# Kernel optimization log

Hardware: AMD Instinct MI355X
Metric: run time of the kernel (lower is better)

The kernel has to match this reference:

```python
import jax, jax.numpy as jnp
import numpy as np

N = 50000      # nodes
E = 800000     # edges (avg degree 16)
IN = 256       # in_features
HD = 4         # num_heads
D = 64         # out_features per head


def setup_inputs() -> dict:
    key = jax.random.key(0)
    k1, k2, k3, k4, k5 = jax.random.split(key, 5)
    h = jax.random.normal(k1, (N, IN), dtype=jnp.float32)
    edge_index = jax.random.randint(k2, (2, E), 0, N)
    # W stored as [in_features, num_heads*out_features] (h @ W == Linear(h))
    W = jax.random.normal(k3, (IN, HD * D), dtype=jnp.float32) * (1.0 / np.sqrt(IN))
    a_src = jax.random.normal(k4, (HD, D), dtype=jnp.float32) * 0.1
    a_dst = jax.random.normal(k5, (HD, D), dtype=jnp.float32) * 0.1
    return {"h": h, "edge_index": edge_index, "W": W, "a_src": a_src, "a_dst": a_dst}


def reference(h, edge_index, W, a_src, a_dst):
    n = h.shape[0]
    src, dst = edge_index[0], edge_index[1]
    # project: [N, H, D]
    hp = (h @ W).reshape(n, HD, D)
    # per-edge attention logits [E, H]
    e_src = jnp.einsum('ehd,hd->eh', hp[src], a_src)
    e_dst = jnp.einsum('ehd,hd->eh', hp[dst], a_dst)
    e = jax.nn.leaky_relu(e_src + e_dst, negative_slope=0.2)
    # segment softmax over incoming edges of each dst node
    e_max = jax.ops.segment_max(e, dst, num_segments=n)          # [N, H]
    ex = jnp.exp(e - e_max[dst])                                  # [E, H]
    e_sum = jax.ops.segment_sum(ex, dst, num_segments=n)         # [N, H]
    alpha = ex / (e_sum[dst] + 1e-16)                             # [E, H]
    # weighted aggregation
    msg = hp[src] * alpha[..., None]                              # [E, H, D]
    out = jax.ops.segment_sum(msg, dst, num_segments=n)          # [N, H, D]
    return out.reshape(n, HD * D)                                 # concat=True
```

## Files before the change

### kernel.cpp

```cpp
#include <hip/hip_runtime.h>

#define HD 4
#define D 64
#define NHD 256
#define N_IN 256

typedef __attribute__((ext_vector_type(8))) __bf16 bf16x8;
typedef __attribute__((ext_vector_type(4))) __bf16 bf16x4;
typedef __attribute__((ext_vector_type(4))) float f32x4;

constexpr int AROW = 40;

__global__ __launch_bounds__(256) void pre_kernel(const float* __restrict__ W,
                                                  __bf16* __restrict__ Wt,
                                                  const int* __restrict__ ei,
                                                  int* __restrict__ deg8, int Nn, int E) {
  const int b = blockIdx.x;
  if (b < N_IN) {
    const int k = b, n = threadIdx.x;
    Wt[n * N_IN + k] = (__bf16)W[k * NHD + n];
  } else {
    const int e = (b - N_IN) * 256 + threadIdx.x;
    const int c = b & 7;
    if (e < E) atomicAdd(&deg8[c * Nn + ei[E + e]], 1);
  }
}

__global__ __launch_bounds__(256) void gemm_scan_kernel(
    const float* __restrict__ A, const __bf16* __restrict__ Wt,
    const float* __restrict__ a_src, const float* __restrict__ a_dst,
    __bf16* __restrict__ hp16, float* __restrict__ s_out, float* __restrict__ t_out,
    int M, const int* __restrict__ deg8, int* __restrict__ partial,
    int* __restrict__ blocksum, int NB, int MT) {
  __shared__ __bf16 As[128 * AROW];
  __shared__ __bf16 Bs[128 * AROW];
  __shared__ int ws4[4];
  const int tid = threadIdx.x;

  if ((int)blockIdx.x < NB) {
    const int lane = tid & 63, wv = tid >> 6;
    const int base = blockIdx.x * 1024 + tid * 4;
    int v[4];
#pragma unroll
    for (int j = 0; j < 4; ++j) {
      int n = base + j;
      int sum = 0;
      if (n < M) {
#pragma unroll
        for (int c = 0; c < 8; ++c) sum += deg8[c * M + n];
      }
      v[j] = sum;
    }
    int sum = v[0] + v[1] + v[2] + v[3];
    int incl = sum;
#pragma unroll
    for (int off = 1; off < 64; off <<= 1) {
      int y = __shfl_up(incl, off);
      if (lane >= off) incl += y;
    }
    if (lane == 63) ws4[wv] = incl;
    __syncthreads();
    int wbase = 0;
#pragma unroll
    for (int w = 0; w < 4; ++w)
      if (w < wv) wbase += ws4[w];
    int excl = wbase + incl - sum;
    if (base + 0 < M) partial[base + 0] = excl;
    if (base + 1 < M) partial[base + 1] = excl + v[0];
    if (base + 2 < M) partial[base + 2] = excl + v[0] + v[1];
    if (base + 3 < M) partial[base + 3] = excl + v[0] + v[1] + v[2];
    if (tid == 255) blocksum[blockIdx.x] = wbase + incl;
    return;
  }

  const int g = blockIdx.x - NB;
  const int bx = g % MT, by = g / MT;
  const int lane = tid & 63, wv = tid >> 6;
  const int wr = wv >> 1, wc = wv & 1;
  const int c15 = lane & 15, quad = lane >> 4;
  const int m0 = bx * 128, n0 = by * 128;

  f32x4 acc[4][4];
#pragma unroll
  for (int i = 0; i < 4; ++i)
#pragma unroll
    for (int j = 0; j < 4; ++j) acc[i][j] = (f32x4){0.f, 0.f, 0.f, 0.f};

  const int am = tid >> 1, aks = (tid & 1) * 16;
  const int gr = m0 + am;
  const bool arow_ok = (gr < M);
  const float* Arow = &A[(size_t)gr * N_IN];
  const __bf16* Brow = &Wt[(size_t)(n0 + am) * N_IN];

  for (int kc = 0; kc < 8; ++kc) {
    const int k0 = kc * 32;
    float4 f0, f1, f2, f3;
    if (arow_ok) {
      f0 = *(const float4*)&Arow[k0 + aks + 0];
      f1 = *(const float4*)&Arow[k0 + aks + 4];
      f2 = *(const float4*)&Arow[k0 + aks + 8];
      f3 = *(const float4*)&Arow[k0 + aks + 12];
    } else {
      f0 = f1 = f2 = f3 = make_float4(0.f, 0.f, 0.f, 0.f);
    }
    bf16x8 b0 = *(const bf16x8*)&Brow[k0 + aks];
    bf16x8 b1 = *(const bf16x8*)&Brow[k0 + aks + 8];

    __syncthreads();
    bf16x8 a0, a1;
    a0[0] = (__bf16)f0.x; a0[1] = (__bf16)f0.y; a0[2] = (__bf16)f0.z; a0[3] = (__bf16)f0.w;
    a0[4] = (__bf16)f1.x; a0[5] = (__bf16)f1.y; a0[6] = (__bf16)f1.z; a0[7] = (__bf16)f1.w;
    a1[0] = (__bf16)f2.x; a1[1] = (__bf16)f2.y; a1[2] = (__bf16)f2.z; a1[3] = (__bf16)f2.w;
    a1[4] = (__bf16)f3.x; a1[5] = (__bf16)f3.y; a1[6] = (__bf16)f3.z; a1[7] = (__bf16)f3.w;
    *(bf16x8*)&As[am * AROW + aks + 0] = a0;
    *(bf16x8*)&As[am * AROW + aks + 8] = a1;
    *(bf16x8*)&Bs[am * AROW + aks + 0] = b0;
    *(bf16x8*)&Bs[am * AROW + aks + 8] = b1;
    __syncthreads();

    bf16x8 af[4], bf_[4];
#pragma unroll
    for (int i = 0; i < 4; ++i) {
      af[i]  = *(bf16x8*)&As[(wr * 64 + i * 16 + c15) * AROW + quad * 8];
      bf_[i] = *(bf16x8*)&Bs[(wc * 64 + i * 16 + c15) * AROW + quad * 8];
    }
#pragma unroll
    for (int mi = 0; mi < 4; ++mi)
#pragma unroll
      for (int ni = 0; ni < 4; ++ni)
        acc[mi][ni] = __builtin_amdgcn_mfma_f32_16x16x32_bf16(af[mi], bf_[ni], acc[mi][ni], 0, 0, 0);
  }

  const int head = by * 2 + wc;
  float av[4], ad[4];
#pragma unroll
  for (int ni = 0; ni < 4; ++ni) {
    av[ni] = a_src[head * D + ni * 16 + c15];
    ad[ni] = a_dst[head * D + ni * 16 + c15];
  }
  const int row0w = m0 + wr * 64;
#pragma unroll
  for (int mi = 0; mi < 4; ++mi) {
#pragma unroll
    for (int j = 0; j < 4; ++j) {
      float ps = acc[mi][0][j] * av[0] + acc[mi][1][j] * av[1] +
                 acc[mi][2][j] * av[2] + acc[mi][3][j] * av[3];
      float pt = acc[mi][0][j] * ad[0] + acc[mi][1][j] * ad[1] +
                 acc[mi][2][j] * ad[2] + acc[mi][3][j] * ad[3];
#pragma unroll
      for (int m = 1; m < 16; m <<= 1) {
        ps += __shfl_xor(ps, m);
        pt += __shfl_xor(pt, m);
      }
      const int row = row0w + mi * 16 + quad * 4 + j;
      if (c15 == 0 && row < M) {
        s_out[row * HD + head] = ps;
        t_out[row * HD + head] = pt;
      }
    }
#pragma unroll
    for (int ni = 0; ni < 4; ++ni) {
#pragma unroll
      for (int j = 0; j < 4; ++j) {
        const int row = row0w + mi * 16 + quad * 4 + j;
        const int col = n0 + wc * 64 + ni * 16 + c15;
        if (row < M) hp16[(size_t)row * NHD + col] = (__bf16)acc[mi][ni][j];
      }
    }
  }
}

__global__ __launch_bounds__(256) void scan23_kernel(const int* __restrict__ partial,
                                                     const int* __restrict__ blocksum,
                                                     const int* __restrict__ deg8,
                                                     int* __restrict__ row_ptr,
                                                     int* __restrict__ cursor8, int n, int NB) {
  __shared__ int s_off;
  const int tid = threadIdx.x;
  if (tid < 64) {
    int v = (tid < NB) ? blocksum[tid] : 0;
    int incl = v;
#pragma unroll
    for (int off = 1; off < 64; off <<= 1) {
      int y = __shfl_up(incl, off);
      if (tid >= off) incl += y;
    }
    int prev = __shfl_up(incl, 1);
    int excl = (tid == 0) ? 0 : prev;
    if (tid == (int)blockIdx.x) s_off = excl;
    if (blockIdx.x == 0 && tid == NB - 1) row_ptr[n] = incl;
  }
  __syncthreads();
  const int off = s_off;
  const int base = blockIdx.x * 1024 + tid * 4;
#pragma unroll
  for (int j = 0; j < 4; ++j) {
    const int node = base + j;
    if (node < n) {
      int rp = partial[node] + off;
      row_ptr[node] = rp;
      int run = rp;
#pragma unroll
      for (int c = 0; c < 8; ++c) {
        cursor8[c * n + node] = run;
        run += deg8[c * n + node];
      }
    }
  }
}

__global__ void scatter_kernel(const int* __restrict__ ei, int* __restrict__ cursor8,
                               int* __restrict__ csr_src, int Nn, int E) {
  int e = blockIdx.x * blockDim.x + threadIdx.x;
  if (e >= E) return;
  const int c = blockIdx.x & 7;
  int sn = ei[e], dn = ei[E + e];
  int pos = atomicAdd(&cursor8[c * Nn + dn], 1);
  csr_src[pos] = sn;
}

__global__ __launch_bounds__(256) void aggregate_kernel(
    const int* __restrict__ row_ptr, const int* __restrict__ csr_src,
    const float* __restrict__ s, const float* __restrict__ t,
    const __bf16* __restrict__ hp16, float* __restrict__ out, int N) {
  const int wave = threadIdx.x >> 6;
  const int lane = threadIdx.x & 63;
  const int node = blockIdx.x * 4 + wave;
  if (node >= N) return;
  const int h = lane >> 4;
  const int d0 = lane * 4;
  const int beg = row_ptr[node], end = row_ptr[node + 1];
  const float tn = t[node * HD + h];
  float num0 = 0.f, num1 = 0.f, num2 = 0.f, num3 = 0.f, den = 0.f;
  int i = beg;
  for (; i + 4 <= end; i += 4) {
    int sn0 = csr_src[i], sn1 = csr_src[i + 1], sn2 = csr_src[i + 2], sn3 = csr_src[i + 3];
    bf16x4 v0 = *(const bf16x4*)&hp16[(size_t)sn0 * NHD + d0];
    bf16x4 v1 = *(const bf16x4*)&hp16[(size_t)sn1 * NHD + d0];
    bf16x4 v2 = *(const bf16x4*)&hp16[(size_t)sn2 * NHD + d0];
    bf16x4 v3 = *(const bf16x4*)&hp16[(size_t)sn3 * NHD + d0];
    float lg0 = s[sn0 * HD + h] + tn;
    float lg1 = s[sn1 * HD + h] + tn;
    float lg2 = s[sn2 * HD + h] + tn;
    float lg3 = s[sn3 * HD + h] + tn;
    lg0 = fmaxf(lg0, 0.2f * lg0);
    lg1 = fmaxf(lg1, 0.2f * lg1);
    lg2 = fmaxf(lg2, 0.2f * lg2);
    lg3 = fmaxf(lg3, 0.2f * lg3);
    float ex0 = __expf(lg0), ex1 = __expf(lg1), ex2 = __expf(lg2), ex3 = __expf(lg3);
    den += (ex0 + ex1) + (ex2 + ex3);
    num0 += ex0 * (float)v0[0] + ex1 * (float)v1[0] + ex2 * (float)v2[0] + ex3 * (float)v3[0];
    num1 += ex0 * (float)v0[1] + ex1 * (float)v1[1] + ex2 * (float)v2[1] + ex3 * (float)v3[1];
    num2 += ex0 * (float)v0[2] + ex1 * (float)v1[2] + ex2 * (float)v2[2] + ex3 * (float)v3[2];
    num3 += ex0 * (float)v0[3] + ex1 * (float)v1[3] + ex2 * (float)v2[3] + ex3 * (float)v3[3];
  }
  for (; i < end; ++i) {
    int sn0 = csr_src[i];
    bf16x4 v0 = *(const bf16x4*)&hp16[(size_t)sn0 * NHD + d0];
    float lg0 = s[sn0 * HD + h] + tn;
    lg0 = fmaxf(lg0, 0.2f * lg0);
    float ex0 = __expf(lg0);
    den += ex0;
    num0 += ex0 * (float)v0[0];
    num1 += ex0 * (float)v0[1];
    num2 += ex0 * (float)v0[2];
    num3 += ex0 * (float)v0[3];
  }
  const float inv = 1.0f / (den + 1e-16f);
  float4 o = make_float4(num0 * inv, num1 * inv, num2 * inv, num3 * inv);
  *(float4*)&out[(size_t)node * NHD + d0] = o;
}

extern "C" void kernel_launch(void* const* d_in, const int* in_sizes, int n_in,
                              void* d_out, int out_size, void* d_ws, size_t ws_size,
                              hipStream_t stream) {
  const float* h_ptr  = (const float*)d_in[0];
  const int*   ei     = (const int*)d_in[1];
  const float* W      = (const float*)d_in[2];
  const float* a_src  = (const float*)d_in[3];
  const float* a_dst  = (const float*)d_in[4];
  float* out = (float*)d_out;

  const int N = in_sizes[0] / N_IN;
  const int E = in_sizes[1] / 2;
  const int NB = (N + 1023) / 1024;
  const int MT = (N + 127) / 128;

  auto align256 = [](size_t x) { return (x + 255) & ~size_t(255); };
  char* base = (char*)d_ws;
  size_t off = 0;
  __bf16* hp16 = (__bf16*)(base + off);  off += align256((size_t)N * NHD * 2);
  __bf16* Wt   = (__bf16*)(base + off);  off += align256((size_t)N_IN * NHD * 2);
  float* s       = (float*)(base + off); off += align256((size_t)N * HD * 4);
  float* t       = (float*)(base + off); off += align256((size_t)N * HD * 4);
  int*   deg8    = (int*)(base + off);   off += align256((size_t)N * 8 * 4);
  int*   cursor8 = (int*)(base + off);   off += align256((size_t)N * 8 * 4);
  int*   partial = (int*)(base + off);   off += align256((size_t)N * 4);
  int*   blocksum= (int*)(base + off);   off += align256((size_t)NB * 4);
  int*   row_ptr = (int*)(base + off);   off += align256((size_t)(N + 1) * 4);
  int*   csr_src = (int*)(base + off);   off += align256((size_t)E * 4);

  hipMemsetAsync(deg8, 0, (size_t)N * 8 * 4, stream);
  pre_kernel<<<N_IN + (E + 255) / 256, 256, 0, stream>>>(W, Wt, ei, deg8, N, E);
  gemm_scan_kernel<<<NB + MT * 2, 256, 0, stream>>>(h_ptr, Wt, a_src, a_dst,
                                                    hp16, s, t, N, deg8, partial,
                                                    blocksum, NB, MT);
  scan23_kernel<<<NB, 256, 0, stream>>>(partial, blocksum, deg8, row_ptr, cursor8, N, NB);
  scatter_kernel<<<(E + 255) / 256, 256, 0, stream>>>(ei, cursor8, csr_src, N, E);
  aggregate_kernel<<<(N + 3) / 4, 256, 0, stream>>>(row_ptr, csr_src, s, t, hp16, out, N);
}
```

Measured before the change: 270.0 us.

## Widen GEMM tile to full 256 columns and unroll aggregation gather by eight

The projection GEMM now uses 512-thread blocks covering all 256 output columns for a 128-row tile. Each fp32 row of h is then read and converted once, where before it was read twice across two column blocks. The scan blocks guard work to the first 256 threads to fit the larger block size. The aggregation loop gains an 8-edge unrolled path so more gathers are in flight per wave, at the cost of more registers.

```diff
diff --git a/kernel.cpp b/kernel.cpp
--- a/kernel.cpp
+++ b/kernel.cpp
@@ -26,59 +26,62 @@
   }
 }
 
-__global__ __launch_bounds__(256) void gemm_scan_kernel(
+__global__ __launch_bounds__(512) void gemm_scan_kernel(
     const float* __restrict__ A, const __bf16* __restrict__ Wt,
     const float* __restrict__ a_src, const float* __restrict__ a_dst,
     __bf16* __restrict__ hp16, float* __restrict__ s_out, float* __restrict__ t_out,
     int M, const int* __restrict__ deg8, int* __restrict__ partial,
     int* __restrict__ blocksum, int NB, int MT) {
   __shared__ __bf16 As[128 * AROW];
-  __shared__ __bf16 Bs[128 * AROW];
+  __shared__ __bf16 Bs[256 * AROW];
   __shared__ int ws4[4];
   const int tid = threadIdx.x;
 
   if ((int)blockIdx.x < NB) {
     const int lane = tid & 63, wv = tid >> 6;
     const int base = blockIdx.x * 1024 + tid * 4;
-    int v[4];
-#pragma unroll
-    for (int j = 0; j < 4; ++j) {
-      int n = base + j;
-      int sum = 0;
-      if (n < M) {
-#pragma unroll
-        for (int c = 0; c < 8; ++c) sum += deg8[c * M + n];
-      }
-      v[j] = sum;
-    }
-    int sum = v[0] + v[1] + v[2] + v[3];
-    int incl = sum;
-#pragma unroll
-    for (int off = 1; off < 64; off <<= 1) {
-      int y = __shfl_up(incl, off);
-      if (lane >= off) incl += y;
-    }
-    if (lane == 63) ws4[wv] = incl;
+    int v[4], sum = 0, incl = 0;
+    if (tid < 256) {
+#pragma unroll
+      for (int j = 0; j < 4; ++j) {
+        int n = base + j;
+        int s = 0;
+        if (n < M) {
+#pragma unroll
+          for (int c = 0; c < 8; ++c) s += deg8[c * M + n];
+        }
+        v[j] = s;
+      }
+      sum = v[0] + v[1] + v[2] + v[3];
+      incl = sum;
+#pragma unroll
+      for (int off = 1; off < 64; off <<= 1) {
+        int y = __shfl_up(incl, off);
+        if (lane >= off) incl += y;
+      }
+      if (lane == 63) ws4[wv] = incl;
+    }
     __syncthreads();
-    int wbase = 0;
-#pragma unroll
-    for (int w = 0; w < 4; ++w)
-      if (w < wv) wbase += ws4[w];
-    int excl = wbase + incl - sum;
-    if (base + 0 < M) partial[base + 0] = excl;
-    if (base + 1 < M) partial[base + 1] = excl + v[0];
-    if (base + 2 < M) partial[base + 2] = excl + v[0] + v[1];
-    if (base + 3 < M) partial[base + 3] = excl + v[0] + v[1] + v[2];
-    if (tid == 255) blocksum[blockIdx.x] = wbase + incl;
+    if (tid < 256) {
+      int wbase = 0;
+#pragma unroll
+      for (int w = 0; w < 4; ++w)
+        if (w < wv) wbase += ws4[w];
+      int excl = wbase + incl - sum;
+      if (base + 0 < M) partial[base + 0] = excl;
+      if (base + 1 < M) partial[base + 1] = excl + v[0];
+      if (base + 2 < M) partial[base + 2] = excl + v[0] + v[1];
+      if (base + 3 < M) partial[base + 3] = excl + v[0] + v[1] + v[2];
+      if (tid == 255) blocksum[blockIdx.x] = wbase + incl;
+    }
     return;
   }
 
   const int g = blockIdx.x - NB;
-  const int bx = g % MT, by = g / MT;
   const int lane = tid & 63, wv = tid >> 6;
-  const int wr = wv >> 1, wc = wv & 1;
+  const int wr = wv >> 2, wc = wv & 3;
   const int c15 = lane & 15, quad = lane >> 4;
-  const int m0 = bx * 128, n0 = by * 128;
+  const int m0 = g * 128;
 
   f32x4 acc[4][4];
 #pragma unroll
@@ -86,36 +89,32 @@
 #pragma unroll
     for (int j = 0; j < 4; ++j) acc[i][j] = (f32x4){0.f, 0.f, 0.f, 0.f};
 
-  const int am = tid >> 1, aks = (tid & 1) * 16;
+  const int am = tid >> 2, aks = (tid & 3) * 8;
   const int gr = m0 + am;
   const bool arow_ok = (gr < M);
   const float* Arow = &A[(size_t)gr * N_IN];
-  const __bf16* Brow = &Wt[(size_t)(n0 + am) * N_IN];
+  const int bm = tid >> 1, bks = (tid & 1) * 16;
+  const __bf16* Brow = &Wt[(size_t)bm * N_IN];
 
   for (int kc = 0; kc < 8; ++kc) {
     const int k0 = kc * 32;
-    float4 f0, f1, f2, f3;
+    float4 f0, f1;
     if (arow_ok) {
       f0 = *(const float4*)&Arow[k0 + aks + 0];
       f1 = *(const float4*)&Arow[k0 + aks + 4];
-      f2 = *(const float4*)&Arow[k0 + aks + 8];
-      f3 = *(const float4*)&Arow[k0 + aks + 12];
     } else {
-      f0 = f1 = f2 = f3 = make_float4(0.f, 0.f, 0.f, 0.f);
-    }
-    bf16x8 b0 = *(const bf16x8*)&Brow[k0 + aks];
-    bf16x8 b1 = *(const bf16x8*)&Brow[k0 + aks + 8];
+      f0 = f1 = make_float4(0.f, 0.f, 0.f, 0.f);
+    }
+    bf16x8 b0 = *(const bf16x8*)&Brow[k0 + bks];
+    bf16x8 b1 = *(const bf16x8*)&Brow[k0 + bks + 8];
 
     __syncthreads();
-    bf16x8 a0, a1;
+    bf16x8 a0;
     a0[0] = (__bf16)f0.x; a0[1] = (__bf16)f0.y; a0[2] = (__bf16)f0.z; a0[3] = (__bf16)f0.w;
     a0[4] = (__bf16)f1.x; a0[5] = (__bf16)f1.y; a0[6] = (__bf16)f1.z; a0[7] = (__bf16)f1.w;
-    a1[0] = (__bf16)f2.x; a1[1] = (__bf16)f2.y; a1[2] = (__bf16)f2.z; a1[3] = (__bf16)f2.w;
-    a1[4] = (__bf16)f3.x; a1[5] = (__bf16)f3.y; a1[6] = (__bf16)f3.z; a1[7] = (__bf16)f3.w;
-    *(bf16x8*)&As[am * AROW + aks + 0] = a0;
-    *(bf16x8*)&As[am * AROW + aks + 8] = a1;
-    *(bf16x8*)&Bs[am * AROW + aks + 0] = b0;
-    *(bf16x8*)&Bs[am * AROW + aks + 8] = b1;
+    *(bf16x8*)&As[am * AROW + aks] = a0;
+    *(bf16x8*)&Bs[bm * AROW + bks] = b0;
+    *(bf16x8*)&Bs[bm * AROW + bks + 8] = b1;
     __syncthreads();
 
     bf16x8 af[4], bf_[4];
@@ -131,7 +130,7 @@
         acc[mi][ni] = __builtin_amdgcn_mfma_f32_16x16x32_bf16(af[mi], bf_[ni], acc[mi][ni], 0, 0, 0);
   }
 
-  const int head = by * 2 + wc;
+  const int head = wc;
   float av[4], ad[4];
 #pragma unroll
   for (int ni = 0; ni < 4; ++ni) {
@@ -163,7 +162,7 @@
 #pragma unroll
       for (int j = 0; j < 4; ++j) {
         const int row = row0w + mi * 16 + quad * 4 + j;
-        const int col = n0 + wc * 64 + ni * 16 + c15;
+        const int col = wc * 64 + ni * 16 + c15;
         if (row < M) hp16[(size_t)row * NHD + col] = (__bf16)acc[mi][ni][j];
       }
     }
@@ -233,6 +232,30 @@
   const float tn = t[node * HD + h];
   float num0 = 0.f, num1 = 0.f, num2 = 0.f, num3 = 0.f, den = 0.f;
   int i = beg;
+  for (; i + 8 <= end; i += 8) {
+    int sn[8];
+#pragma unroll
+    for (int u = 0; u < 8; ++u) sn[u] = csr_src[i + u];
+    bf16x4 v[8];
+#pragma unroll
+    for (int u = 0; u < 8; ++u) v[u] = *(const bf16x4*)&hp16[(size_t)sn[u] * NHD + d0];
+    float lg[8];
+#pragma unroll
+    for (int u = 0; u < 8; ++u) lg[u] = s[sn[u] * HD + h] + tn;
+#pragma unroll
+    for (int u = 0; u < 8; ++u) {
+      lg[u] = fmaxf(lg[u], 0.2f * lg[u]);
+      lg[u] = __expf(lg[u]);
+    }
+#pragma unroll
+    for (int u = 0; u < 8; ++u) {
+      den  += lg[u];
+      num0 += lg[u] * (float)v[u][0];
+      num1 += lg[u] * (float)v[u][1];
+      num2 += lg[u] * (float)v[u][2];
+      num3 += lg[u] * (float)v[u][3];
+    }
+  }
   for (; i + 4 <= end; i += 4) {
     int sn0 = csr_src[i], sn1 = csr_src[i + 1], sn2 = csr_src[i + 2], sn3 = csr_src[i + 3];
     bf16x4 v0 = *(const bf16x4*)&hp16[(size_t)sn0 * NHD + d0];
@@ -302,9 +325,9 @@
 
   hipMemsetAsync(deg8, 0, (size_t)N * 8 * 4, stream);
   pre_kernel<<<N_IN + (E + 255) / 256, 256, 0, stream>>>(W, Wt, ei, deg8, N, E);
-  gemm_scan_kernel<<<NB + MT * 2, 256, 0, stream>>>(h_ptr, Wt, a_src, a_dst,
-                                                    hp16, s, t, N, deg8, partial,
-                                                    blocksum, NB, MT);
+  gemm_scan_kernel<<<NB + MT, 512, 0, stream>>>(h_ptr, Wt, a_src, a_dst,
+                                                hp16, s, t, N, deg8, partial,
+                                                blocksum, NB, MT);
   scan23_kernel<<<NB, 256, 0, stream>>>(partial, blocksum, deg8, row_ptr, cursor8, N, NB);
   scatter_kernel<<<(E + 255) / 256, 256, 0, stream>>>(ei, cursor8, csr_src, N, E);
   aggregate_kernel<<<(N + 3) / 4, 256, 0, stream>>>(row_ptr, csr_src, s, t, hp16, out, N);
```

New measurement: 275.1 us. About the same (+1.9%).

## Scatter edges into channel-major buckets then permute into dst-sorted CSR

Applied to the files above, without the earlier changes.

The CSR build now computes eight separate per-channel prefix scans, so each channel's cursors form contiguous regions. The scatter kernel writes into these channel-major buckets, which improves locality of the atomic cursor updates and the writes. A new permute kernel then uses per-block binary search to remap every entry into the final dst-sorted csr_src. The cost is an extra kernel launch, an extra E-sized buffer with a full read and write pass, and more scan work.

```diff
diff --git a/kernel.cpp b/kernel.cpp
--- a/kernel.cpp
+++ b/kernel.cpp
@@ -4,6 +4,7 @@
 #define D 64
 #define NHD 256
 #define N_IN 256
+#define NPB 128
 
 typedef __attribute__((ext_vector_type(8))) __bf16 bf16x8;
 typedef __attribute__((ext_vector_type(4))) __bf16 bf16x4;
@@ -30,8 +31,8 @@
     const float* __restrict__ A, const __bf16* __restrict__ Wt,
     const float* __restrict__ a_src, const float* __restrict__ a_dst,
     __bf16* __restrict__ hp16, float* __restrict__ s_out, float* __restrict__ t_out,
-    int M, const int* __restrict__ deg8, int* __restrict__ partial,
-    int* __restrict__ blocksum, int NB, int MT) {
+    int M, const int* __restrict__ deg8, int* __restrict__ partial8,
+    int* __restrict__ blocksum8, int NB, int MT) {
   __shared__ __bf16 As[128 * AROW];
   __shared__ __bf16 Bs[128 * AROW];
   __shared__ int ws4[4];
@@ -40,36 +41,39 @@
   if ((int)blockIdx.x < NB) {
     const int lane = tid & 63, wv = tid >> 6;
     const int base = blockIdx.x * 1024 + tid * 4;
-    int v[4];
-#pragma unroll
-    for (int j = 0; j < 4; ++j) {
-      int n = base + j;
-      int sum = 0;
-      if (n < M) {
-#pragma unroll
-        for (int c = 0; c < 8; ++c) sum += deg8[c * M + n];
-      }
-      v[j] = sum;
-    }
-    int sum = v[0] + v[1] + v[2] + v[3];
-    int incl = sum;
-#pragma unroll
-    for (int off = 1; off < 64; off <<= 1) {
-      int y = __shfl_up(incl, off);
-      if (lane >= off) incl += y;
-    }
-    if (lane == 63) ws4[wv] = incl;
-    __syncthreads();
-    int wbase = 0;
-#pragma unroll
-    for (int w = 0; w < 4; ++w)
-      if (w < wv) wbase += ws4[w];
-    int excl = wbase + incl - sum;
-    if (base + 0 < M) partial[base + 0] = excl;
-    if (base + 1 < M) partial[base + 1] = excl + v[0];
-    if (base + 2 < M) partial[base + 2] = excl + v[0] + v[1];
-    if (base + 3 < M) partial[base + 3] = excl + v[0] + v[1] + v[2];
-    if (tid == 255) blocksum[blockIdx.x] = wbase + incl;
+#pragma unroll 1
+    for (int c = 0; c < 8; ++c) {
+      int v0 = 0, v1 = 0, v2 = 0, v3 = 0;
+      if (base + 3 < M) {
+        int4 q = *(const int4*)&deg8[c * M + base];
+        v0 = q.x; v1 = q.y; v2 = q.z; v3 = q.w;
+      } else {
+        if (base + 0 < M) v0 = deg8[c * M + base + 0];
+        if (base + 1 < M) v1 = deg8[c * M + base + 1];
+        if (base + 2 < M) v2 = deg8[c * M + base + 2];
+        if (base + 3 < M) v3 = deg8[c * M + base + 3];
+      }
+      const int sum = v0 + v1 + v2 + v3;
+      int incl = sum;
+#pragma unroll
+      for (int off = 1; off < 64; off <<= 1) {
+        int y = __shfl_up(incl, off);
+        if (lane >= off) incl += y;
+      }
+      if (lane == 63) ws4[wv] = incl;
+      __syncthreads();
+      int wbase = 0;
+#pragma unroll
+      for (int w = 0; w < 4; ++w)
+        if (w < wv) wbase += ws4[w];
+      __syncthreads();
+      const int excl = wbase + incl - sum;
+      if (base + 0 < M) partial8[c * M + base + 0] = excl;
+      if (base + 1 < M) partial8[c * M + base + 1] = excl + v0;
+      if (base + 2 < M) partial8[c * M + base + 2] = excl + v0 + v1;
+      if (base + 3 < M) partial8[c * M + base + 3] = excl + v0 + v1 + v2;
+      if (tid == 255) blocksum8[c * NB + blockIdx.x] = wbase + incl;
+    }
     return;
   }
 
@@ -170,53 +174,109 @@
   }
 }
 
-__global__ __launch_bounds__(256) void scan23_kernel(const int* __restrict__ partial,
-                                                     const int* __restrict__ blocksum,
-                                                     const int* __restrict__ deg8,
-                                                     int* __restrict__ row_ptr,
-                                                     int* __restrict__ cursor8, int n, int NB) {
-  __shared__ int s_off;
+__global__ __launch_bounds__(256) void scan23_kernel(
+    const int* __restrict__ partial8, const int* __restrict__ blocksum8,
+    int* __restrict__ row_ptr, int* __restrict__ pcur0, int* __restrict__ cursor8,
+    int n, int NB) {
+  __shared__ int s_choff[8], s_B[8], s_T[8];
   const int tid = threadIdx.x;
   if (tid < 64) {
-    int v = (tid < NB) ? blocksum[tid] : 0;
-    int incl = v;
-#pragma unroll
-    for (int off = 1; off < 64; off <<= 1) {
-      int y = __shfl_up(incl, off);
-      if (tid >= off) incl += y;
-    }
-    int prev = __shfl_up(incl, 1);
-    int excl = (tid == 0) ? 0 : prev;
-    if (tid == (int)blockIdx.x) s_off = excl;
-    if (blockIdx.x == 0 && tid == NB - 1) row_ptr[n] = incl;
+    int runB = 0;
+#pragma unroll 1
+    for (int c = 0; c < 8; ++c) {
+      int v = (tid < NB) ? blocksum8[c * NB + tid] : 0;
+      int incl = v;
+#pragma unroll
+      for (int off = 1; off < 64; off <<= 1) {
+        int y = __shfl_up(incl, off);
+        if (tid >= off) incl += y;
+      }
+      const int excl = incl - v;
+      const int choff = __shfl(excl, (int)blockIdx.x);
+      const int Tc = __shfl(incl, NB - 1);
+      if (tid == 0) { s_choff[c] = choff; s_B[c] = runB; s_T[c] = Tc; }
+      runB += Tc;
+    }
+    if (blockIdx.x == 0 && tid == 0) row_ptr[n] = runB;
   }
   __syncthreads();
-  const int off = s_off;
+  if (blockIdx.x == 0 && tid < 8)
+    pcur0[tid * (n + 1) + n] = s_B[tid] + s_T[tid];
   const int base = blockIdx.x * 1024 + tid * 4;
-#pragma unroll
-  for (int j = 0; j < 4; ++j) {
-    const int node = base + j;
-    if (node < n) {
-      int rp = partial[node] + off;
-      row_ptr[node] = rp;
-      int run = rp;
-#pragma unroll
-      for (int c = 0; c < 8; ++c) {
-        cursor8[c * n + node] = run;
-        run += deg8[c * n + node];
-      }
-    }
-  }
+  int rp0 = 0, rp1 = 0, rp2 = 0, rp3 = 0;
+  const bool full = (base + 3 < n);
+#pragma unroll 1
+  for (int c = 0; c < 8; ++c) {
+    int p0 = 0, p1 = 0, p2 = 0, p3 = 0;
+    if (full) {
+      int4 q = *(const int4*)&partial8[c * n + base];
+      p0 = q.x; p1 = q.y; p2 = q.z; p3 = q.w;
+    } else {
+      if (base + 0 < n) p0 = partial8[c * n + base + 0];
+      if (base + 1 < n) p1 = partial8[c * n + base + 1];
+      if (base + 2 < n) p2 = partial8[c * n + base + 2];
+    }
+    const int ch = s_choff[c], bB = s_B[c];
+    if (base + 0 < n) { int P = ch + p0, pc = bB + P; pcur0[c*(n+1)+base+0] = pc; cursor8[c*n+base+0] = pc; rp0 += P; }
+    if (base + 1 < n) { int P = ch + p1, pc = bB + P; pcur0[c*(n+1)+base+1] = pc; cursor8[c*n+base+1] = pc; rp1 += P; }
+    if (base + 2 < n) { int P = ch + p2, pc = bB + P; pcur0[c*(n+1)+base+2] = pc; cursor8[c*n+base+2] = pc; rp2 += P; }
+    if (base + 3 < n) { int P = ch + p3, pc = bB + P; pcur0[c*(n+1)+base+3] = pc; cursor8[c*n+base+3] = pc; rp3 += P; }
+  }
+  if (base + 0 < n) row_ptr[base + 0] = rp0;
+  if (base + 1 < n) row_ptr[base + 1] = rp1;
+  if (base + 2 < n) row_ptr[base + 2] = rp2;
+  if (base + 3 < n) row_ptr[base + 3] = rp3;
 }
 
 __global__ void scatter_kernel(const int* __restrict__ ei, int* __restrict__ cursor8,
-                               int* __restrict__ csr_src, int Nn, int E) {
+                               int* __restrict__ tmp_src, int Nn, int E) {
   int e = blockIdx.x * blockDim.x + threadIdx.x;
   if (e >= E) return;
   const int c = blockIdx.x & 7;
   int sn = ei[e], dn = ei[E + e];
   int pos = atomicAdd(&cursor8[c * Nn + dn], 1);
-  csr_src[pos] = sn;
+  tmp_src[pos] = sn;
+}
+
+__global__ __launch_bounds__(256) void permute_kernel(
+    const int* __restrict__ pcur0, const int* __restrict__ row_ptr,
+    const int* __restrict__ tmp_src, int* __restrict__ csr_src, int n) {
+  __shared__ int spc[8][NPB + 1];
+  __shared__ int sO[8][NPB];
+  __shared__ int srp[NPB];
+  const int tid = threadIdx.x;
+  const int n0 = blockIdx.x * NPB;
+  const int cnt = (n - n0 < NPB) ? (n - n0) : NPB;
+  for (int idx = tid; idx < 8 * (NPB + 1); idx += 256) {
+    const int c = idx / (NPB + 1), i = idx - c * (NPB + 1);
+    int ni = n0 + i; if (ni > n) ni = n;
+    spc[c][i] = pcur0[c * (n + 1) + ni];
+  }
+  for (int i = tid; i < cnt; i += 256) srp[i] = row_ptr[n0 + i];
+  __syncthreads();
+  for (int i = tid; i < cnt; i += 256) {
+    int run = 0;
+#pragma unroll
+    for (int c = 0; c < 8; ++c) { sO[c][i] = run; run += spc[c][i + 1] - spc[c][i]; }
+  }
+  __syncthreads();
+  const int lane = tid & 63, wv = tid >> 6;
+#pragma unroll 1
+  for (int c = wv; c < 8; c += 4) {
+    const int S = spc[c][0];
+    const int L = spc[c][cnt] - S;
+    for (int k = lane; k < L; k += 64) {
+      const int q = S + k;
+      const int val = tmp_src[q];
+      int lo = 0, hi = cnt;
+      while (hi - lo > 1) {
+        const int mid = (lo + hi) >> 1;
+        if (spc[c][mid] <= q) lo = mid; else hi = mid;
+      }
+      const int dest = srp[lo] + sO[c][lo] + (q - spc[c][lo]);
+      csr_src[dest] = val;
+    }
+  }
 }
 
 __global__ __launch_bounds__(256) void aggregate_kernel(
@@ -291,21 +351,24 @@
   size_t off = 0;
   __bf16* hp16 = (__bf16*)(base + off);  off += align256((size_t)N * NHD * 2);
   __bf16* Wt   = (__bf16*)(base + off);  off += align256((size_t)N_IN * NHD * 2);
-  float* s       = (float*)(base + off); off += align256((size_t)N * HD * 4);
-  float* t       = (float*)(base + off); off += align256((size_t)N * HD * 4);
-  int*   deg8    = (int*)(base + off);   off += align256((size_t)N * 8 * 4);
-  int*   cursor8 = (int*)(base + off);   off += align256((size_t)N * 8 * 4);
-  int*   partial = (int*)(base + off);   off += align256((size_t)N * 4);
-  int*   blocksum= (int*)(base + off);   off += align256((size_t)NB * 4);
-  int*   row_ptr = (int*)(base + off);   off += align256((size_t)(N + 1) * 4);
-  int*   csr_src = (int*)(base + off);   off += align256((size_t)E * 4);
+  float* s        = (float*)(base + off); off += align256((size_t)N * HD * 4);
+  float* t        = (float*)(base + off); off += align256((size_t)N * HD * 4);
+  int*   deg8     = (int*)(base + off);   off += align256((size_t)N * 8 * 4);
+  int*   cursor8  = (int*)(base + off);   off += align256((size_t)N * 8 * 4);
+  int*   partial8 = (int*)(base + off);   off += align256((size_t)N * 8 * 4);
+  int*   blocksum8= (int*)(base + off);   off += align256((size_t)NB * 8 * 4);
+  int*   row_ptr  = (int*)(base + off);   off += align256((size_t)(N + 1) * 4);
+  int*   pcur0    = (int*)(base + off);   off += align256((size_t)(N + 1) * 8 * 4);
+  int*   tmp_src  = (int*)(base + off);   off += align256((size_t)E * 4);
+  int*   csr_src  = (int*)(base + off);   off += align256((size_t)E * 4);
 
   hipMemsetAsync(deg8, 0, (size_t)N * 8 * 4, stream);
   pre_kernel<<<N_IN + (E + 255) / 256, 256, 0, stream>>>(W, Wt, ei, deg8, N, E);
   gemm_scan_kernel<<<NB + MT * 2, 256, 0, stream>>>(h_ptr, Wt, a_src, a_dst,
-                                                    hp16, s, t, N, deg8, partial,
-                                                    blocksum, NB, MT);
-  scan23_kernel<<<NB, 256, 0, stream>>>(partial, blocksum, deg8, row_ptr, cursor8, N, NB);
-  scatter_kernel<<<(E + 255) / 256, 256, 0, stream>>>(ei, cursor8, csr_src, N, E);
+                                                    hp16, s, t, N, deg8, partial8,
+                                                    blocksum8, NB, MT);
+  scan23_kernel<<<NB, 256, 0, stream>>>(partial8, blocksum8, row_ptr, pcur0, cursor8, N, NB);
+  scatter_kernel<<<(E + 255) / 256, 256, 0, stream>>>(ei, cursor8, tmp_src, N, E);
+  permute_kernel<<<(N + NPB - 1) / NPB, 256, 0, stream>>>(pcur0, row_ptr, tmp_src, csr_src, N);
   aggregate_kernel<<<(N + 3) / 4, 256, 0, stream>>>(row_ptr, csr_src, s, t, hp16, out, N);
 }
```

Measured after the change: 282.9 us. 4.8% more time.
